# Performance work log

Hardware: AMD Instinct MI355X
Metric: run time of the kernel (lower is better)

Reference implementation:

```python
import jax, jax.numpy as jnp
import numpy as np

EMB = 384
HID = 256
HEADS = 4
HD = HID // HEADS  # 64
LAYERS = 2
M_DOCS = 32
TOTAL = 4096  # 1 query + 32 docs + 4063 sentences
LN_EPS = 1e-5


def _layernorm(x, scale, bias):
    mu = jnp.mean(x, axis=-1, keepdims=True)
    var = jnp.mean(jnp.square(x - mu), axis=-1, keepdims=True)
    return (x - mu) * jax.lax.rsqrt(var + LN_EPS) * scale + bias


def setup_inputs() -> dict:
    key = jax.random.key(0)
    ks = jax.random.split(key, 12)
    g = 0.05  # small init scale (stand-in for xavier)
    return {
        "node_embeddings": jax.random.normal(ks[0], (TOTAL, EMB), jnp.float32),
        "adj": jax.random.randint(ks[1], (TOTAL, TOTAL), 0, 2, jnp.int32),
        "num_docs": M_DOCS,
        "proj_w": jax.random.normal(ks[2], (HID, EMB), jnp.float32) * g,
        "proj_b": jnp.zeros((HID,), jnp.float32),
        "ln_scale": jnp.ones((LAYERS, HID), jnp.float32),
        "ln_bias": jnp.zeros((LAYERS, HID), jnp.float32),
        "gat_W": jax.random.normal(ks[3], (LAYERS, HEADS, HD, HID), jnp.float32) * g,
        "gat_a": jax.random.normal(ks[4], (LAYERS, HEADS, 2 * HD), jnp.float32) * g,
        "fusion_w": jax.random.normal(ks[5], (HID, 2 * HID + 2), jnp.float32) * g,
        "fusion_b": jnp.zeros((HID,), jnp.float32),
        "out_w": jax.random.normal(ks[6], (HID,), jnp.float32) * g,
        "out_b": jnp.float32(0.5),
    }


def reference(node_embeddings, adj, num_docs, proj_w, proj_b, ln_scale, ln_bias,
              gat_W, gat_a, fusion_w, fusion_b, out_w, out_b):
    T = node_embeddings.shape[0]
    M = num_docs
    N = T - 1 - M  # number of sentences
    # input projection + relu (dropout = identity in eval)
    h = jax.nn.relu(node_embeddings @ proj_w.T + proj_b)  # (T, HID)
    # query-guided sentence re-weighting
    q = h[0:1]                     # (1, HID)
    s = h[1 + M:]                  # (N, HID)
    qn = q / (jnp.linalg.norm(q, axis=1, keepdims=True) + 1e-8)
    sn = s / (jnp.linalg.norm(s, axis=1, keepdims=True) + 1e-8)
    cos = (qn @ sn.T).reshape(-1, 1)          # (N,1)
    s = s + 0.8 * q * cos
    h = jnp.concatenate([h[:1 + M], s], axis=0)
    mask = (adj == 0)[None]                   # (1,T,T)
    for i in range(LAYERS):
        res = h
        x = _layernorm(h, ln_scale[i], ln_bias[i])
        Wh = jnp.einsum('nd,hkd->hnk', x, gat_W[i])                # (H,T,HD)
        # concat-attention a.[Wh_i ; Wh_j] == a_src.Wh_i + a_dst.Wh_j
        src = jnp.einsum('hnk,hk->hn', Wh, gat_a[i, :, :HD])       # (H,T)
        dst = jnp.einsum('hnk,hk->hn', Wh, gat_a[i, :, HD:])       # (H,T)
        e = jax.nn.leaky_relu(src[:, :, None] + dst[:, None, :], 0.2)  # (H,T,T)
        e = jnp.where(mask, -jnp.inf, e)
        attn = jax.nn.softmax(e, axis=-1)                          # softmax over j
        hn = jnp.einsum('hij,hjk->hik', attn, Wh)                  # (H,T,HD)
        hcat = jnp.transpose(hn, (1, 0, 2)).reshape(T, HEADS * HD)
        h = 0.5 * jax.nn.relu(hcat) + 0.5 * res
    qh = h[0:1]
    sh = h[1 + M:]
    scores = (qh @ sh.T) / (HID ** 0.5)       # (1,N)
    aw = jax.nn.softmax(scores, axis=-1)
    awT = aw.T                                # (N,1)
    qw = qh * (awT + 0.5)                     # (N,HID)
    qnf = qh / (jnp.linalg.norm(qh, axis=1, keepdims=True) + 1e-8)
    snf = sh / (jnp.linalg.norm(sh, axis=1, keepdims=True) + 1e-8)
    cosf = (qnf @ snf.T).reshape(-1, 1)       # (N,1)
    feat = jnp.concatenate([sh, qw, cosf, awT], axis=1)  # (N, 2*HID+2)
    g = jax.nn.relu(feat @ fusion_w.T + fusion_b)
    out = g @ out_w + out_b                   # (N,)
    return out + 0.5 * cosf[:, 0]
```

## Files before the change

kernel.cpp:

```cpp
#include <hip/hip_runtime.h>
#include <hip/hip_bf16.h>
#include <stdint.h>

#define TOTAL 4096
#define EMB 384
#define MD 32
#define NDOCS (TOTAL - 1 - MD)
#define LN_EPS 1e-5f
#define NEGF (-1e30f)

typedef __hip_bfloat16 bf16;
typedef unsigned short ushort_t;
typedef __attribute__((ext_vector_type(8))) short short8;
typedef __attribute__((ext_vector_type(4))) float f32x4;
typedef __attribute__((ext_vector_type(2))) float f32x2;

__device__ __forceinline__ float ldf(const void* p, int i, int isbf) {
    return isbf ? __bfloat162float(((const bf16*)p)[i]) : ((const float*)p)[i];
}

__device__ __forceinline__ unsigned f2bf(float x) {
    return (__float_as_uint(x) + 0x8000u) >> 16;
}

__device__ __forceinline__ unsigned fenc(float f) {
    unsigned u = __float_as_uint(f);
    return (u >> 31) ? ~u : (u | 0x80000000u);
}
__device__ __forceinline__ float fdec(unsigned k) {
    return __uint_as_float((k & 0x80000000u) ? (k & 0x7FFFFFFFu) : ~k);
}

#define TRTOT (EMB * 256 + 2 * 65536 + 514 * 256)
__global__ __launch_bounds__(256) void k_adjmask(
        const int* adj, unsigned long long* maskb,
        const uint16_t* embp, int* flag, unsigned* dmaxu,
        const void* proj_w, const void* proj_b, const void* gat_W,
        const void* fusion_w,
        float* projT, float* gatT, float* fwT, float* qrow) {
    __shared__ int red[4];
    __shared__ float qred2[4];
    int bid = blockIdx.x, t = threadIdx.x;
    int w = t >> 6, l = t & 63;
#pragma unroll
    for (int r8 = 0; r8 < 8; r8++) {
        int i = bid * 8 + r8;
        for (int c = w; c < 64; c += 4) {
            int a = adj[(size_t)i * TOTAL + c * 64 + l];
            unsigned long long m = __ballot(a != 0);
            if (l == 0) maskb[i * 64 + c] = m;
        }
    }
    if (bid == 0) {
        for (int idx = t; idx < 2048; idx += 256) dmaxu[idx] = 0x007FFFFFu;
    }
    int cnt = 0;
    for (int k = t; k < 4096; k += 256) {
        uint16_t wd = embp[2 * k];
        int e = (wd >> 7) & 0xFF;
        if (e >= 100 && e <= 140) cnt++;
    }
    for (int o = 32; o > 0; o >>= 1) cnt += __shfl_down(cnt, o);
    if ((t & 63) == 0) red[t >> 6] = cnt;
    __syncthreads();
    int isbf = (red[0] + red[1] + red[2] + red[3] > 2048) ? 1 : 0;
    if (bid == 0 && t == 0) flag[0] = isbf;
    for (int idx = bid * 256 + t; idx < TRTOT; idx += 512 * 256) {
        if (idx < EMB * 256) {
            int d = idx >> 8, c = idx & 255;
            projT[(d >> 2) * 1024 + c * 4 + (d & 3)] = ldf(proj_w, c * EMB + d, isbf);
        } else if (idx < EMB * 256 + 2 * 65536) {
            int r = idx - EMB * 256;
            int ll = r >> 16, rem = r & 65535;
            int d = rem >> 8, c = rem & 255;
            gatT[ll * 65536 + (d >> 2) * 1024 + c * 4 + (d & 3)] =
                ldf(gat_W, ll * 65536 + c * 256 + d, isbf);
        } else {
            int r = idx - (EMB * 256 + 2 * 65536);
            int j = r >> 8, c = r & 255;
            fwT[(j >> 2) * 1024 + c * 4 + (j & 3)] = ldf(fusion_w, c * 514 + j, isbf);
        }
    }
    if (bid == 511) {
        const void* embv = (const void*)embp;
        float p0 = 0.f, p1 = 0.f, p2 = 0.f, p3 = 0.f;
#pragma unroll 4
        for (int d = 0; d < EMB; d += 4) {
            float e0 = ldf(embv, d, isbf),     e1 = ldf(embv, d + 1, isbf);
            float e2 = ldf(embv, d + 2, isbf), e3 = ldf(embv, d + 3, isbf);
            p0 = fmaf(e0, ldf(proj_w, (size_t)t * EMB + d, isbf), p0);
            p1 = fmaf(e1, ldf(proj_w, (size_t)t * EMB + d + 1, isbf), p1);
            p2 = fmaf(e2, ldf(proj_w, (size_t)t * EMB + d + 2, isbf), p2);
            p3 = fmaf(e3, ldf(proj_w, (size_t)t * EMB + d + 3, isbf), p3);
        }
        float accq = (p0 + p2) + (p1 + p3);
        float qv = fmaxf(accq + ldf(proj_b, t, isbf), 0.f);
        qrow[t] = qv;
        float a = qv * qv;
        for (int o = 32; o > 0; o >>= 1) a += __shfl_down(a, o);
        if ((t & 63) == 0) qred2[t >> 6] = a;
        __syncthreads();
        if (t == 0) qrow[256] = sqrtf(qred2[0] + qred2[1] + qred2[2] + qred2[3]) + 1e-8f;
    }
}

#define LR 8
__global__ __launch_bounds__(512) void k_lnwh(
        const void* emb, const void* proj_b, const float* projT,
        float* h, const float* gatT, const void* ln_scale, const void* ln_bias,
        const void* gat_a, ushort_t* whswz, float* srcb, unsigned* d12g,
        unsigned* dmaxu, int layer, const int* flagp, const float* qrow) {
    __shared__ float embs[8][EMB];
    __shared__ float xs[8][256];
    __shared__ float xpart[8][4][256];
    int isbf = flagp[0];
    int t5 = threadIdx.x;
    int w8 = t5 >> 6;
    int l = t5 & 63;
    int i0 = blockIdx.x * LR;
    int myrow = i0 + w8;
    float hv[4];
    if (layer == 0) {
        for (int idx = t5; idx < 8 * EMB; idx += 512) {
            int r = idx / EMB, d = idx % EMB;
            embs[r][d] = ldf(emb, (i0 + r) * EMB + d, isbf);
        }
        __syncthreads();
        const float4* pT4 = (const float4*)projT;
        float ap[8][4];
#pragma unroll
        for (int r = 0; r < 8; r++)
#pragma unroll
            for (int cc = 0; cc < 4; cc++) ap[r][cc] = 0.f;
        for (int s = 0; s < 12; s++) {
            int k4 = w8 * 12 + s;
            float4 wv[4];
#pragma unroll
            for (int cc = 0; cc < 4; cc++) wv[cc] = pT4[k4 * 256 + cc * 64 + l];
#pragma unroll
            for (int r = 0; r < 8; r++) {
                float4 x = *(const float4*)&embs[r][k4 * 4];
#pragma unroll
                for (int cc = 0; cc < 4; cc++) {
                    ap[r][cc] = fmaf(x.x, wv[cc].x, ap[r][cc]);
                    ap[r][cc] = fmaf(x.y, wv[cc].y, ap[r][cc]);
                    ap[r][cc] = fmaf(x.z, wv[cc].z, ap[r][cc]);
                    ap[r][cc] = fmaf(x.w, wv[cc].w, ap[r][cc]);
                }
            }
        }
#pragma unroll
        for (int r = 0; r < 4; r++)
#pragma unroll
            for (int cc = 0; cc < 4; cc++) xpart[w8][r][cc * 64 + l] = ap[r][cc];
        __syncthreads();
        float bias[4];
#pragma unroll
        for (int cc = 0; cc < 4; cc++) bias[cc] = ldf(proj_b, cc * 64 + l, isbf);
        if (w8 < 4) {
#pragma unroll
            for (int cc = 0; cc < 4; cc++) {
                float s = 0.f;
#pragma unroll
                for (int g = 0; g < 8; g++) s += xpart[g][w8][cc * 64 + l];
                hv[cc] = fmaxf(s + bias[cc], 0.f);
            }
        }
        __syncthreads();
#pragma unroll
        for (int r = 4; r < 8; r++)
#pragma unroll
            for (int cc = 0; cc < 4; cc++) xpart[w8][r - 4][cc * 64 + l] = ap[r][cc];
        __syncthreads();
        if (w8 >= 4) {
#pragma unroll
            for (int cc = 0; cc < 4; cc++) {
                float s = 0.f;
#pragma unroll
                for (int g = 0; g < 8; g++) s += xpart[g][w8 - 4][cc * 64 + l];
                hv[cc] = fmaxf(s + bias[cc], 0.f);
            }
        }
        if (myrow >= 1 + MD) {
            float qv[4];
#pragma unroll
            for (int cc = 0; cc < 4; cc++) qv[cc] = qrow[cc * 64 + l];
            float b = 0.f, c = 0.f;
#pragma unroll
            for (int cc = 0; cc < 4; cc++) {
                b = fmaf(hv[cc], hv[cc], b);
                c = fmaf(qv[cc], hv[cc], c);
            }
            for (int o = 32; o > 0; o >>= 1) { b += __shfl_xor(b, o); c += __shfl_xor(c, o); }
            float qn = qrow[256];
            float k = 0.8f * (c / (qn * (sqrtf(b) + 1e-8f)));
#pragma unroll
            for (int cc = 0; cc < 4; cc++) hv[cc] += k * qv[cc];
        }
#pragma unroll
        for (int cc = 0; cc < 4; cc++) h[(size_t)myrow * 256 + cc * 64 + l] = hv[cc];
    } else {
#pragma unroll
        for (int cc = 0; cc < 4; cc++) hv[cc] = h[(size_t)myrow * 256 + cc * 64 + l];
    }
    {
        float a = 0.f, b2 = 0.f;
#pragma unroll
        for (int cc = 0; cc < 4; cc++) { a += hv[cc]; b2 = fmaf(hv[cc], hv[cc], b2); }
        for (int o = 32; o > 0; o >>= 1) { a += __shfl_xor(a, o); b2 += __shfl_xor(b2, o); }
        float mu = a * (1.f / 256.f);
        float var = b2 * (1.f / 256.f) - mu * mu;
        float rs = rsqrtf(var + LN_EPS);
#pragma unroll
        for (int cc = 0; cc < 4; cc++) {
            float sc = ldf(ln_scale, layer * 256 + cc * 64 + l, isbf);
            float lb = ldf(ln_bias, layer * 256 + cc * 64 + l, isbf);
            xs[w8][cc * 64 + l] = (hv[cc] - mu) * rs * sc + lb;
        }
    }
    __syncthreads();
    const float4* gT4 = (const float4*)(gatT + layer * 65536);
    float aw[8][4];
#pragma unroll
    for (int r = 0; r < 8; r++)
#pragma unroll
        for (int cc = 0; cc < 4; cc++) aw[r][cc] = 0.f;
    for (int s = 0; s < 8; s++) {
        int k4 = w8 * 8 + s;
        float4 wv[4];
#pragma unroll
        for (int cc = 0; cc < 4; cc++) wv[cc] = gT4[k4 * 256 + cc * 64 + l];
#pragma unroll
        for (int r = 0; r < 8; r++) {
            float4 x = *(const float4*)&xs[r][k4 * 4];
#pragma unroll
            for (int cc = 0; cc < 4; cc++) {
                aw[r][cc] = fmaf(x.x, wv[cc].x, aw[r][cc]);
                aw[r][cc] = fmaf(x.y, wv[cc].y, aw[r][cc]);
                aw[r][cc] = fmaf(x.z, wv[cc].z, aw[r][cc]);
                aw[r][cc] = fmaf(x.w, wv[cc].w, aw[r][cc]);
            }
        }
    }
#pragma unroll
    for (int r = 0; r < 4; r++)
#pragma unroll
        for (int cc = 0; cc < 4; cc++) xpart[w8][r][cc * 64 + l] = aw[r][cc];
    __syncthreads();
    float acc2[4];
    if (w8 < 4) {
#pragma unroll
        for (int cc = 0; cc < 4; cc++) {
            float s = 0.f;
#pragma unroll
            for (int g = 0; g < 8; g++) s += xpart[g][w8][cc * 64 + l];
            acc2[cc] = s;
        }
    }
    __syncthreads();
#pragma unroll
    for (int r = 4; r < 8; r++)
#pragma unroll
        for (int cc = 0; cc < 4; cc++) xpart[w8][r - 4][cc * 64 + l] = aw[r][cc];
    __syncthreads();
    if (w8 >= 4) {
#pragma unroll
        for (int cc = 0; cc < 4; cc++) {
            float s = 0.f;
#pragma unroll
            for (int g = 0; g < 8; g++) s += xpart[g][w8 - 4][cc * 64 + l];
            acc2[cc] = s;
        }
    }
#pragma unroll
    for (int cc = 0; cc < 4; cc++) {
        int col = cc * 64 + l;
        int off = (myrow >> 6) * 16384 + (col >> 6) * 4096 + ((myrow >> 3) & 7) * 512 +
                  ((col >> 4) & 3) * 128 + (col & 15) * 8 + (myrow & 7);
        whswz[off] = (ushort_t)f2bf(acc2[cc]);
    }
    float sv[4], dv[4];
#pragma unroll
    for (int cc = 0; cc < 4; cc++) {
        float av1 = ldf(gat_a, layer * 512 + cc * 128 + l, isbf);
        float av2 = ldf(gat_a, layer * 512 + cc * 128 + 64 + l, isbf);
        sv[cc] = acc2[cc] * av1;
        dv[cc] = acc2[cc] * av2;
    }
    for (int o = 32; o > 0; o >>= 1) {
#pragma unroll
        for (int cc = 0; cc < 4; cc++) {
            sv[cc] += __shfl_down(sv[cc], o);
            dv[cc] += __shfl_down(dv[cc], o);
        }
    }
    if (l == 0) {
        const float LOG2E = 1.44269504f;
#pragma unroll
        for (int cc = 0; cc < 4; cc++) {
            srcb[cc * 4096 + myrow] = sv[cc];
            float D1 = exp2f(dv[cc] * LOG2E), D2 = exp2f(0.2f * dv[cc] * LOG2E);
            d12g[cc * 4096 + myrow] = (f2bf(D2) << 16) | f2bf(D1);
            atomicMax(&dmaxu[(blockIdx.x & 63) * 16 + cc], fenc(dv[cc]));
        }
    }
}

#define TI 16
__global__ __launch_bounds__(512) void k_pv(const ushort_t* whswz, const float* srcb,
                                            const unsigned* dmaxu, const unsigned* d12g,
                                            const unsigned long long* maskb, float* h) {
    __shared__ unsigned long long mbs[16 * 66];
    __shared__ __align__(16) f32x4 accsh[16 * 64];
    __shared__ __align__(16) float lsh[4][4][4];
    __shared__ float srcs[64];
    __shared__ float dmx[4];
    __shared__ unsigned mlut[4];
    int t = threadIdx.x;
    int W = t >> 6, lane = t & 63;
    int hH = W & 3, kq = W >> 2;
    int quad = lane >> 4, c16 = lane & 15;
    int i0 = blockIdx.x * TI;
    if (t < 4) mlut[t] = (t & 1 ? 0x0000FFFFu : 0u) | (t & 2 ? 0xFFFF0000u : 0u);
    if (t < 256) {
        int hh = t >> 6, sl = t & 63;
        float v = fdec(dmaxu[sl * 16 + hh]);
        for (int o = 32; o > 0; o >>= 1) v = fmaxf(v, __shfl_xor(v, o));
        if (sl == 0) dmx[hh] = v;
    }
    for (int idx = t; idx < 16 * 64; idx += 512) {
        int r = idx >> 6, wd = idx & 63;
        mbs[r * 66 + wd] = maskb[(size_t)(i0 + r) * 64 + wd];
    }
    if (t < 64) srcs[t] = srcb[(t >> 4) * 4096 + i0 + (t & 15)];
    __syncthreads();
    const float LOG2E = 1.44269504f;
    float dm = dmx[hH];
    float src = srcs[hH * 16 + c16];
    float sd = src + dm;
    float rce = -fmaxf(sd, 0.2f * sd);
    float E1 = exp2f((src + rce) * LOG2E);
    float E2 = exp2f((0.2f * src + rce) * LOG2E);
    f32x4 acc[4];
    f32x4 accl = (f32x4){0.f, 0.f, 0.f, 0.f};
#pragma unroll
    for (int ct = 0; ct < 4; ct++) acc[ct] = (f32x4){0.f, 0.f, 0.f, 0.f};
    uint4 onesu;
    unsigned os = (c16 == 0) ? 0x3F803F80u : 0u;
    onesu.x = os; onesu.y = os; onesu.z = os; onesu.w = os;
    short8 bfones = __builtin_bit_cast(short8, onesu);
    const uint4* g4 = (const uint4*)whswz;
    const uint4* d4 = (const uint4*)d12g;
    size_t b0 = (size_t)hH * 512 + (size_t)(kq * 4 + quad) * 64 + c16;
    int dbase = hH * 1024, d0i = kq * 8 + quad * 2;
    uint4 bA0 = g4[b0],        bA1 = g4[b0 + 16],        bA2 = g4[b0 + 32],        bA3 = g4[b0 + 48];
    uint4 bB0 = g4[b0 + 2048], bB1 = g4[b0 + 2048 + 16], bB2 = g4[b0 + 2048 + 32], bB3 = g4[b0 + 2048 + 48];
    uint4 dA0 = d4[dbase + d0i],      dA1 = d4[dbase + d0i + 1];
    uint4 dB0 = d4[dbase + 16 + d0i], dB1 = d4[dbase + 16 + d0i + 1];
    auto pvstep = [&](uint4& B0, uint4& B1, uint4& B2, uint4& B3,
                      uint4& DD0, uint4& DD1, int s) {
        uint4 bc0 = B0, bc1 = B1, bc2 = B2, bc3 = B3;
        uint4 dc0 = DD0, dc1 = DD1;
        if (s < 62) {
            size_t bs = b0 + (size_t)(s + 2) * 2048;
            B0 = g4[bs]; B1 = g4[bs + 16]; B2 = g4[bs + 32]; B3 = g4[bs + 48];
            int di = dbase + (s + 2) * 16 + d0i;
            DD0 = d4[di]; DD1 = d4[di + 1];
        }
        unsigned mby = (unsigned)(mbs[c16 * 66 + s] >> (kq * 32 + quad * 8)) & 0xFFu;
        unsigned dw[8] = {dc0.x, dc0.y, dc0.z, dc0.w, dc1.x, dc1.y, dc1.z, dc1.w};
        unsigned pu[4];
#pragma unroll
        for (int q = 0; q < 4; q++) {
            unsigned a = dw[2 * q], b = dw[2 * q + 1];
            f32x2 D1 = (f32x2){__uint_as_float(a << 16), __uint_as_float(b << 16)};
            f32x2 D2 = (f32x2){__uint_as_float(a & 0xFFFF0000u), __uint_as_float(b & 0xFFFF0000u)};
            f32x2 v1 = D1 * E1;
            f32x2 v2 = D2 * E2;
            f32x2 m = __builtin_elementwise_max(v1, v2);
            unsigned v = ((__float_as_uint(m.x) + 0x8000u) >> 16) |
                         ((__float_as_uint(m.y) + 0x8000u) & 0xFFFF0000u);
            pu[q] = v & mlut[(mby >> (2 * q)) & 3u];
        }
        uint4 afu;
        afu.x = pu[0]; afu.y = pu[1]; afu.z = pu[2]; afu.w = pu[3];
        short8 af = __builtin_bit_cast(short8, afu);
        acc[0] = __builtin_amdgcn_mfma_f32_16x16x32_bf16(af, __builtin_bit_cast(short8, bc0), acc[0], 0, 0, 0);
        acc[1] = __builtin_amdgcn_mfma_f32_16x16x32_bf16(af, __builtin_bit_cast(short8, bc1), acc[1], 0, 0, 0);
        acc[2] = __builtin_amdgcn_mfma_f32_16x16x32_bf16(af, __builtin_bit_cast(short8, bc2), acc[2], 0, 0, 0);
        acc[3] = __builtin_amdgcn_mfma_f32_16x16x32_bf16(af, __builtin_bit_cast(short8, bc3), acc[3], 0, 0, 0);
        accl = __builtin_amdgcn_mfma_f32_16x16x32_bf16(af, bfones, accl, 0, 0, 0);
    };
    for (int sp = 0; sp < 32; sp++) {
        pvstep(bA0, bA1, bA2, bA3, dA0, dA1, 2 * sp);
        pvstep(bB0, bB1, bB2, bB3, dB0, dB1, 2 * sp + 1);
    }
    __syncthreads();
    if (kq == 1) {
#pragma unroll
        for (int ct = 0; ct < 4; ct++)
            accsh[(hH * 4 + ct) * 64 + lane] = acc[ct];
        if (c16 == 0) *(f32x4*)&lsh[hH][quad][0] = accl;
    }
    __syncthreads();
    if (kq == 0) {
        float ls[4];
#pragma unroll
        for (int rr = 0; rr < 4; rr++)
            ls[rr] = __shfl(accl[rr], quad * 16) + lsh[hH][quad][rr];
#pragma unroll
        for (int ct = 0; ct < 4; ct++) {
            f32x4 o = acc[ct] + accsh[(hH * 4 + ct) * 64 + lane];
#pragma unroll
            for (int rr = 0; rr < 4; rr++) {
                int row = i0 + quad * 4 + rr;
                size_t idx = (size_t)row * 256 + hH * 64 + ct * 16 + c16;
                float hn = 0.5f * fmaxf(o[rr] / ls[rr], 0.f) + 0.5f * h[idx];
                h[idx] = hn;
            }
        }
    }
}

__global__ __launch_bounds__(256) void k_scores(const float* h, float* scoresv, float* cosv,
                                                float* swp) {
    int t = threadIdx.x, W = t >> 6, lane = t & 63;
    const float4* h4 = (const float4*)h;
    int gw = blockIdx.x * 4 + W;
    float4 q4 = h4[lane];
    float a = q4.x * q4.x + q4.y * q4.y + q4.z * q4.z + q4.w * q4.w;
    for (int o = 32; o > 0; o >>= 1) a += __shfl_xor(a, o);
    float qn = sqrtf(a) + 1e-8f;
    float mw = NEGF, sw = 0.f;
    for (int n = gw; n < NDOCS; n += 1024) {
        float4 s4 = h4[(size_t)(1 + MD + n) * 64 + lane];
        float b = s4.x * s4.x + s4.y * s4.y + s4.z * s4.z + s4.w * s4.w;
        float c = q4.x * s4.x + q4.y * s4.y + q4.z * s4.z + q4.w * s4.w;
        for (int o = 32; o > 0; o >>= 1) { b += __shfl_xor(b, o); c += __shfl_xor(c, o); }
        float sc = c * (1.f / 16.f);
        if (lane == 0) {
            scoresv[n] = sc;
            cosv[n] = c / (qn * (sqrtf(b) + 1e-8f));
        }
        float mn = fmaxf(mw, sc);
        sw = sw * __expf(mw - mn) + __expf(sc - mn);
        mw = mn;
    }
    if (lane == 0) { swp[2 * gw] = mw; swp[2 * gw + 1] = sw; }
}

#define TN 8
__global__ __launch_bounds__(256) void k_fusion(const float* h,
                                                const float* scoresv, const float* swp,
                                                const float* cosv,
                                                const float* fwT, const void* fusion_b,
                                                const void* out_w, const void* out_bp,
                                                void* outv, const int* flagp) {
    __shared__ float feats2[514][TN];
    __shared__ float qhs[256];
    __shared__ float red[TN][4];
    __shared__ float reds[2][4];
    __shared__ float aws[TN];
    int isbf = flagp[0];
    int t = threadIdx.x;
    int n0 = blockIdx.x * TN;
    qhs[t] = h[t];
    float M = NEGF, S = 0.f;
    for (int idx = t; idx < 1024; idx += 256) {
        float pm = swp[2 * idx], ps = swp[2 * idx + 1];
        float mn = fmaxf(M, pm);
        S = S * __expf(M - mn) + ps * __expf(pm - mn);
        M = mn;
    }
    for (int o = 32; o > 0; o >>= 1) {
        float m2 = __shfl_xor(M, o), s2 = __shfl_xor(S, o);
        float mn = fmaxf(M, m2);
        S = S * __expf(M - mn) + s2 * __expf(m2 - mn);
        M = mn;
    }
    if ((t & 63) == 0) { reds[0][t >> 6] = M; reds[1][t >> 6] = S; }
    __syncthreads();
    float Mf = fmaxf(fmaxf(reds[0][0], reds[0][1]), fmaxf(reds[0][2], reds[0][3]));
    float Sf = reds[1][0] * __expf(reds[0][0] - Mf) + reds[1][1] * __expf(reds[0][1] - Mf) +
               reds[1][2] * __expf(reds[0][2] - Mf) + reds[1][3] * __expf(reds[0][3] - Mf);
    float invS = 1.f / Sf;
    if (t < TN) {
        int n = n0 + t;
        aws[t] = (n < NDOCS) ? __expf(scoresv[n] - Mf) * invS : 0.f;
    }
    __syncthreads();
    for (int idx = t; idx < 514 * TN; idx += 256) {
        int j = idx >> 3, r = idx & 7;
        int n = n0 + r;
        float v = 0.f;
        if (n < NDOCS) {
            if (j < 256) v = h[(size_t)(1 + MD + n) * 256 + j];
            else if (j < 512) v = qhs[j - 256] * (aws[r] + 0.5f);
            else if (j == 512) v = cosv[n];
            else v = aws[r];
        }
        feats2[j][r] = v;
    }
    __syncthreads();
    float acc[TN];
    float bk = ldf(fusion_b, t, isbf);
#pragma unroll
    for (int r = 0; r < TN; r++) acc[r] = bk;
    const float4* fT4 = (const float4*)fwT;
    for (int j0 = 0; j0 < 512; j0 += 8) {
        float4 wa = fT4[(j0 >> 2) * 256 + t];
        float4 wb = fT4[((j0 >> 2) + 1) * 256 + t];
        float wv[8] = {wa.x, wa.y, wa.z, wa.w, wb.x, wb.y, wb.z, wb.w};
#pragma unroll
        for (int u = 0; u < 8; u++) {
            float4 fa = *(const float4*)&feats2[j0 + u][0];
            float4 fb = *(const float4*)&feats2[j0 + u][4];
            acc[0] = fmaf(fa.x, wv[u], acc[0]); acc[1] = fmaf(fa.y, wv[u], acc[1]);
            acc[2] = fmaf(fa.z, wv[u], acc[2]); acc[3] = fmaf(fa.w, wv[u], acc[3]);
            acc[4] = fmaf(fb.x, wv[u], acc[4]); acc[5] = fmaf(fb.y, wv[u], acc[5]);
            acc[6] = fmaf(fb.z, wv[u], acc[6]); acc[7] = fmaf(fb.w, wv[u], acc[7]);
        }
    }
    {
        float4 wt = fT4[128 * 256 + t];
#pragma unroll
        for (int r = 0; r < TN; r++) acc[r] = fmaf(feats2[512][r], wt.x, acc[r]);
#pragma unroll
        for (int r = 0; r < TN; r++) acc[r] = fmaf(feats2[513][r], wt.y, acc[r]);
    }
    float ow = ldf(out_w, t, isbf);
    float outb = ldf(out_bp, 0, isbf);
#pragma unroll
    for (int r = 0; r < TN; r++) {
        float o = fmaxf(acc[r], 0.f) * ow;
        for (int off = 32; off > 0; off >>= 1) o += __shfl_down(o, off);
        if ((t & 63) == 0) red[r][t >> 6] = o;
    }
    __syncthreads();
    if (t < TN) {
        int n = n0 + t;
        if (n < NDOCS) {
            float o = red[t][0] + red[t][1] + red[t][2] + red[t][3] + outb + 0.5f * cosv[n];
            if (isbf) ((bf16*)outv)[n] = __float2bfloat16(o);
            else      ((float*)outv)[n] = o;
        }
    }
}

extern "C" void kernel_launch(void* const* d_in, const int* in_sizes, int n_in,
                              void* d_out, int out_size, void* d_ws, size_t ws_size,
                              hipStream_t stream) {
    const void* emb      = d_in[0];
    const int*  adj      = (const int*)d_in[1];
    const void* proj_w   = d_in[3];
    const void* proj_b   = d_in[4];
    const void* ln_scale = d_in[5];
    const void* ln_bias  = d_in[6];
    const void* gat_W    = d_in[7];
    const void* gat_a    = d_in[8];
    const void* fusion_w = d_in[9];
    const void* fusion_b = d_in[10];
    const void* out_w    = d_in[11];
    const void* out_b    = d_in[12];

    unsigned long long* maskb = (unsigned long long*)d_ws;
    int* flag = (int*)((char*)d_ws + (size_t)4096 * 64 * 8);
    float* f = (float*)((char*)d_ws + (size_t)4096 * 64 * 8 + 256);
    float* h       = f; f += 4096 * 256;
    float* srcb    = f; f += 4 * 4096;
    unsigned* d12g = (unsigned*)f; f += 4 * 4096;
    unsigned* dmaxu = (unsigned*)f; f += 2048;
    float* projT   = f; f += EMB * 256;
    float* gatT    = f; f += 2 * 65536;
    float* fwT     = f; f += 129 * 1024;
    float* scoresv = f; f += 4096;
    float* cosv    = f; f += 4096;
    float* swpart  = f; f += 2048;
    float* qrowb   = f; f += 260;
    ushort_t* whswz = (ushort_t*)f; f += 4096 * 256 / 2;

    k_adjmask<<<dim3(512), dim3(256), 0, stream>>>(adj, maskb, (const uint16_t*)emb, flag,
                                                   dmaxu, proj_w, proj_b, gat_W, fusion_w,
                                                   projT, gatT, fwT, qrowb);
    for (int layer = 0; layer < 2; layer++) {
        k_lnwh<<<dim3(TOTAL / LR), dim3(512), 0, stream>>>(emb, proj_b, projT, h, gatT,
                                                           ln_scale, ln_bias, gat_a,
                                                           whswz, srcb, d12g,
                                                           dmaxu + layer * 1024, layer, flag,
                                                           qrowb);
        k_pv<<<dim3(TOTAL / TI), dim3(512), 0, stream>>>(whswz, srcb, dmaxu + layer * 1024,
                                                         d12g, maskb, h);
    }
    k_scores<<<dim3(256), dim3(256), 0, stream>>>(h, scoresv, cosv, swpart);
    k_fusion<<<dim3((NDOCS + TN - 1) / TN), dim3(256), 0, stream>>>(h, scoresv, swpart,
                                                                    cosv, fwT, fusion_b, out_w,
                                                                    out_b, (void*)d_out, flag);
}
```

Measured before the change: 367.3 us.

## Vectorize adjacency bitmask build and give one block per row

The preprocessing kernel now launches one block per adjacency row plus one extra block. Each thread reads adjacency as int4 and builds 64-bit masks with shuffle-or reductions instead of scalar loads and ballots. The weight transposes now read the source coalesced and scatter the writes. The query-row projection moves to a dedicated block that stages the embedding in shared memory and uses vector weight loads. The aim is more memory parallelism on the 64 MB adjacency read and removing the slow serial tail of the old query block, at the cost of every block redoing the dtype-detection scan.

After: 317.0 us. 1.16x faster.

```diff
diff --git a/kernel.cpp b/kernel.cpp
--- a/kernel.cpp
+++ b/kernel.cpp
@@ -40,20 +40,9 @@
         float* projT, float* gatT, float* fwT, float* qrow) {
     __shared__ int red[4];
     __shared__ float qred2[4];
+    __shared__ float embs[EMB];
     int bid = blockIdx.x, t = threadIdx.x;
     int w = t >> 6, l = t & 63;
-#pragma unroll
-    for (int r8 = 0; r8 < 8; r8++) {
-        int i = bid * 8 + r8;
-        for (int c = w; c < 64; c += 4) {
-            int a = adj[(size_t)i * TOTAL + c * 64 + l];
-            unsigned long long m = __ballot(a != 0);
-            if (l == 0) maskb[i * 64 + c] = m;
-        }
-    }
-    if (bid == 0) {
-        for (int idx = t; idx < 2048; idx += 256) dmaxu[idx] = 0x007FFFFFu;
-    }
     int cnt = 0;
     for (int k = t; k < 4096; k += 256) {
         uint16_t wd = embp[2 * k];
@@ -65,33 +54,75 @@
     __syncthreads();
     int isbf = (red[0] + red[1] + red[2] + red[3] > 2048) ? 1 : 0;
     if (bid == 0 && t == 0) flag[0] = isbf;
-    for (int idx = bid * 256 + t; idx < TRTOT; idx += 512 * 256) {
+    if (bid < 4096) {
+        const int4* adj4 = (const int4*)(adj + (size_t)bid * TOTAL);
+        unsigned long long parts[4];
+#pragma unroll
+        for (int it = 0; it < 4; it++) {
+            int4 a = adj4[it * 256 + t];
+            unsigned nib = (a.x != 0 ? 1u : 0u) | (a.y != 0 ? 2u : 0u) |
+                           (a.z != 0 ? 4u : 0u) | (a.w != 0 ? 8u : 0u);
+            parts[it] = (unsigned long long)nib << (4 * (l & 15));
+        }
+#pragma unroll
+        for (int it = 0; it < 4; it++) {
+            unsigned long long m = parts[it];
+            m |= __shfl_xor(m, 1);
+            m |= __shfl_xor(m, 2);
+            m |= __shfl_xor(m, 4);
+            m |= __shfl_xor(m, 8);
+            if ((l & 15) == 0)
+                maskb[bid * 64 + it * 16 + w * 4 + (l >> 4)] = m;
+        }
+        if (bid == 0) {
+            for (int idx = t; idx < 2048; idx += 256) dmaxu[idx] = 0x007FFFFFu;
+        }
+        int idx = bid * 256 + t;
         if (idx < EMB * 256) {
-            int d = idx >> 8, c = idx & 255;
-            projT[(d >> 2) * 1024 + c * 4 + (d & 3)] = ldf(proj_w, c * EMB + d, isbf);
+            int c = idx / EMB, d = idx - c * EMB;
+            projT[(d >> 2) * 1024 + c * 4 + (d & 3)] = ldf(proj_w, idx, isbf);
         } else if (idx < EMB * 256 + 2 * 65536) {
             int r = idx - EMB * 256;
             int ll = r >> 16, rem = r & 65535;
-            int d = rem >> 8, c = rem & 255;
-            gatT[ll * 65536 + (d >> 2) * 1024 + c * 4 + (d & 3)] =
-                ldf(gat_W, ll * 65536 + c * 256 + d, isbf);
+            int c = rem >> 8, d = rem & 255;
+            gatT[ll * 65536 + (d >> 2) * 1024 + c * 4 + (d & 3)] = ldf(gat_W, r, isbf);
+        } else if (idx < TRTOT) {
+            int r = idx - (EMB * 256 + 2 * 65536);
+            int c = r / 514, j = r - c * 514;
+            fwT[(j >> 2) * 1024 + c * 4 + (j & 3)] = ldf(fusion_w, r, isbf);
+        }
+    } else {
+        for (int d = t; d < EMB; d += 256) embs[d] = ldf((const void*)embp, d, isbf);
+        __syncthreads();
+        float p0 = 0.f, p1 = 0.f, p2 = 0.f, p3 = 0.f;
+        if (!isbf) {
+            const float4* W4 = (const float4*)proj_w;
+#pragma unroll 8
+            for (int k = 0; k < 96; k++) {
+                float4 wv = W4[t * 96 + k];
+                float4 e = *(const float4*)&embs[k * 4];
+                p0 = fmaf(e.x, wv.x, p0); p1 = fmaf(e.y, wv.y, p1);
+                p2 = fmaf(e.z, wv.z, p2); p3 = fmaf(e.w, wv.w, p3);
+            }
         } else {
-            int r = idx - (EMB * 256 + 2 * 65536);
-            int j = r >> 8, c = r & 255;
-            fwT[(j >> 2) * 1024 + c * 4 + (j & 3)] = ldf(fusion_w, c * 514 + j, isbf);
-        }
-    }
-    if (bid == 511) {
-        const void* embv = (const void*)embp;
-        float p0 = 0.f, p1 = 0.f, p2 = 0.f, p3 = 0.f;
-#pragma unroll 4
-        for (int d = 0; d < EMB; d += 4) {
-            float e0 = ldf(embv, d, isbf),     e1 = ldf(embv, d + 1, isbf);
-            float e2 = ldf(embv, d + 2, isbf), e3 = ldf(embv, d + 3, isbf);
-            p0 = fmaf(e0, ldf(proj_w, (size_t)t * EMB + d, isbf), p0);
-            p1 = fmaf(e1, ldf(proj_w, (size_t)t * EMB + d + 1, isbf), p1);
-            p2 = fmaf(e2, ldf(proj_w, (size_t)t * EMB + d + 2, isbf), p2);
-            p3 = fmaf(e3, ldf(proj_w, (size_t)t * EMB + d + 3, isbf), p3);
+            const uint4* W4 = (const uint4*)proj_w;
+#pragma unroll 8
+            for (int k = 0; k < 48; k++) {
+                uint4 raw = W4[t * 48 + k];
+                unsigned rws[4] = {raw.x, raw.y, raw.z, raw.w};
+#pragma unroll
+                for (int q = 0; q < 4; q++) {
+                    float we = __uint_as_float(rws[q] << 16);
+                    float wo = __uint_as_float(rws[q] & 0xFFFF0000u);
+                    if ((q & 1) == 0) {
+                        p0 = fmaf(embs[k * 8 + 2 * q], we, p0);
+                        p1 = fmaf(embs[k * 8 + 2 * q + 1], wo, p1);
+                    } else {
+                        p2 = fmaf(embs[k * 8 + 2 * q], we, p2);
+                        p3 = fmaf(embs[k * 8 + 2 * q + 1], wo, p3);
+                    }
+                }
+            }
         }
         float accq = (p0 + p2) + (p1 + p3);
         float qv = fmaxf(accq + ldf(proj_b, t, isbf), 0.f);
@@ -579,9 +610,9 @@
     float* qrowb   = f; f += 260;
     ushort_t* whswz = (ushort_t*)f; f += 4096 * 256 / 2;
 
-    k_adjmask<<<dim3(512), dim3(256), 0, stream>>>(adj, maskb, (const uint16_t*)emb, flag,
-                                                   dmaxu, proj_w, proj_b, gat_W, fusion_w,
-                                                   projT, gatT, fwT, qrowb);
+    k_adjmask<<<dim3(4097), dim3(256), 0, stream>>>(adj, maskb, (const uint16_t*)emb, flag,
+                                                    dmaxu, proj_w, proj_b, gat_W, fusion_w,
+                                                    projT, gatT, fwT, qrowb);
     for (int layer = 0; layer < 2; layer++) {
         k_lnwh<<<dim3(TOTAL / LR), dim3(512), 0, stream>>>(emb, proj_b, projT, h, gatT,
                                                            ln_scale, ln_bias, gat_a,
```
